# Kernel tuning notes

Hardware: AMD Instinct MI355X
Metric: run time of the kernel (lower is better)

The kernel has to match this reference:

```python
import jax, jax.numpy as jnp
import numpy as np

EPS = 1e-6
NUM_HEADS = 16


def _layernorm(x, g, b):
    m = jnp.mean(x, axis=-1, keepdims=True)
    v = jnp.mean(jnp.square(x - m), axis=-1, keepdims=True)
    return (x - m) * jax.lax.rsqrt(v + EPS) * g + b


def setup_inputs() -> dict:
    key = jax.random.key(0)
    ks = jax.random.split(key, 16)
    B, Lq, Lkv, D = 2, 2048, 4096, 2048
    Hd = D // NUM_HEADS
    s = 0.02
    return {
        "hidden_states": jax.random.normal(ks[0], (B, Lq, D), jnp.float32),
        "cross_attention_states": jax.random.normal(ks[1], (B, Lkv, D), jnp.float32),
        "q_w": jax.random.normal(ks[2], (D, D), jnp.float32) * s,
        "q_b": jnp.zeros((D,), jnp.float32),
        "k_w": jax.random.normal(ks[3], (D, D), jnp.float32) * s,
        "k_b": jnp.zeros((D,), jnp.float32),
        "v_w": jax.random.normal(ks[4], (D, D), jnp.float32) * s,
        "v_b": jnp.zeros((D,), jnp.float32),
        "o_w": jax.random.normal(ks[5], (D, D), jnp.float32) * s,
        "o_b": jnp.zeros((D,), jnp.float32),
        "qn_g": jnp.ones((Hd,), jnp.float32),
        "qn_b": jnp.zeros((Hd,), jnp.float32),
        "kn_g": jnp.ones((Hd,), jnp.float32),
        "kn_b": jnp.zeros((Hd,), jnp.float32),
    }


def reference(hidden_states, cross_attention_states,
              q_w, q_b, k_w, k_b, v_w, v_b, o_w, o_b,
              qn_g, qn_b, kn_g, kn_b):
    B, Lq, D = hidden_states.shape
    H = NUM_HEADS
    Hd = D // H
    scale = Hd ** -0.5

    # torch Linear: y = x @ W^T + b
    q = hidden_states @ q_w.T + q_b                        # [B,Lq,D]
    k = cross_attention_states @ k_w.T + k_b               # [B,Lkv,D]
    v = cross_attention_states @ v_w.T + v_b               # [B,Lkv,D]

    q = q.reshape(B, Lq, H, Hd).transpose(0, 2, 1, 3)      # [B,H,Lq,Hd]
    k = k.reshape(B, -1, H, Hd).transpose(0, 2, 1, 3)      # [B,H,Lkv,Hd]
    v = v.reshape(B, -1, H, Hd).transpose(0, 2, 1, 3)      # [B,H,Lkv,Hd]

    # per-head QK LayerNorm before scores
    q = _layernorm(q, qn_g, qn_b)
    k = _layernorm(k, kn_g, kn_b)

    attn_weights = jnp.einsum('bhqd,bhkd->bhqk', q, k) * scale
    attn_weights = jax.nn.softmax(attn_weights.astype(jnp.float32), axis=-1).astype(q.dtype)
    # dropout p=0.0 (inference) -> identity

    attn_output = jnp.einsum('bhqk,bhkd->bhqd', attn_weights, v)
    attn_output = attn_output.transpose(0, 2, 1, 3).reshape(B, Lq, D)
    attn_output = attn_output @ o_w.T + o_b
    return attn_output, attn_weights
```

## Files before the change

### kernel.cpp

```cpp
#include <hip/hip_runtime.h>
#include <cstdint>
#include <cstddef>

using u16 = unsigned short;
using f32x4 = __attribute__((ext_vector_type(4))) float;
using bf8   = __attribute__((ext_vector_type(8))) short;
using u32x4 = __attribute__((ext_vector_type(4))) unsigned;

#define DEVFN __device__ __forceinline__

constexpr int BB  = 2;
constexpr int LQ  = 2048;
constexpr int LKV = 4096;
constexpr int DD  = 2048;
constexpr int NH  = 16;
constexpr int HDm = 128;
constexpr float ATTN_SCALE = 0.08838834764831845f;
constexpr float LN_EPS = 1e-6f;
constexpr float LOG2E  = 1.4426950408889634f;
constexpr float SHIFT2 = 17.312340490667562f;

DEVFN u16 f2bf(float f) {
  unsigned u = __builtin_bit_cast(unsigned, f);
  u += 0x7fffu + ((u >> 16) & 1u);
  return (u16)(u >> 16);
}
DEVFN float bf2f(u16 h) { return __builtin_bit_cast(float, (unsigned)h << 16); }
DEVFN f32x4 mfma16(bf8 a, bf8 b, f32x4 c) {
  return __builtin_amdgcn_mfma_f32_16x16x32_bf16(a, b, c, 0, 0, 0);
}
DEVFN void gl16(const void* g, void* l) {
  __builtin_amdgcn_global_load_lds(
      (const __attribute__((address_space(1))) void*)g,
      (__attribute__((address_space(3))) void*)l, 16, 0, 0);
}
DEVFN void barrier_hard() {
  __builtin_amdgcn_s_barrier();
  __builtin_amdgcn_sched_barrier(0);
}

struct C6 {
  const float4* s[6];
  ushort4* d[6];
  unsigned off[7];
};
__global__ __launch_bounds__(256) void k_cvt6(C6 a) {
  unsigned gi = blockIdx.x * 256 + threadIdx.x;
  if (gi >= a.off[6]) return;
  int seg = 0;
#pragma unroll
  for (int i = 1; i < 6; ++i) seg += (gi >= a.off[i]);
  unsigned j = gi - a.off[seg];
  float4 v = a.s[seg][j];
  ushort4 o;
  o.x = f2bf(v.x); o.y = f2bf(v.y); o.z = f2bf(v.z); o.w = f2bf(v.w);
  a.d[seg][j] = o;
}

template <int MODE>
DEVFN void gemm_body(const u16* __restrict__ X, const u16* __restrict__ Wt,
                     const float* __restrict__ bias,
                     const float* __restrict__ lng, const float* __restrict__ lnb,
                     void* __restrict__ Y, int M, int N, int K,
                     int m0, int n0, u16* Sh, float (*Sm)[128], float (*Sq)[128]) {
  u16* As = Sh;
  u16* Bs = Sh + 128 * 64;
  const int tid = threadIdx.x;
  const int w = tid >> 6, l = tid & 63;
  const int wr = w >> 1, wc = w & 1;
  const int lr = l & 15, lk = (l >> 4) * 8;
  const int rsw = (l & 7) << 3;
  const int srow = l >> 3;
  const int scb = (l & 7) * 16;
  f32x4 acc[4][4] = {};

  for (int k0 = 0; k0 < K; k0 += 64) {
#pragma unroll
    for (int i = 0; i < 4; ++i) {
      int rbase = w * 32 + i * 8;
      int row = rbase + srow;
      int cb = scb ^ ((row & 7) << 4);
      gl16((const char*)&X[(size_t)(m0 + row) * K + k0] + cb, &As[rbase * 64]);
      gl16((const char*)&Wt[(size_t)(n0 + row) * K + k0] + cb, &Bs[rbase * 64]);
    }
    __syncthreads();
    bf8 af[4][2], bfr[4][2];
#pragma unroll
    for (int mi = 0; mi < 4; ++mi)
#pragma unroll
      for (int kk = 0; kk < 2; ++kk)
        af[mi][kk] = *(const bf8*)&As[(wr * 64 + mi * 16 + lr) * 64 + ((kk * 32 + lk) ^ rsw)];
#pragma unroll
    for (int ni = 0; ni < 4; ++ni)
#pragma unroll
      for (int kk = 0; kk < 2; ++kk)
        bfr[ni][kk] = *(const bf8*)&Bs[(wc * 64 + ni * 16 + lr) * 64 + ((kk * 32 + lk) ^ rsw)];
#pragma unroll
    for (int kk = 0; kk < 2; ++kk)
#pragma unroll
      for (int mi = 0; mi < 4; ++mi)
#pragma unroll
        for (int ni = 0; ni < 4; ++ni)
          acc[mi][ni] = mfma16(af[mi][kk], bfr[ni][kk], acc[mi][ni]);
    __syncthreads();
  }
  const int lrg = (l >> 4) * 4;

  float bv[4];
#pragma unroll
  for (int ni = 0; ni < 4; ++ni) bv[ni] = bias[n0 + wc * 64 + ni * 16 + lr];
#pragma unroll
  for (int mi = 0; mi < 4; ++mi)
#pragma unroll
    for (int ni = 0; ni < 4; ++ni)
#pragma unroll
      for (int r = 0; r < 4; ++r) acc[mi][ni][r] += bv[ni];

  if constexpr (MODE == 2 || MODE == 3) {
#pragma unroll
    for (int mi = 0; mi < 4; ++mi) {
#pragma unroll
      for (int r = 0; r < 4; ++r) {
        float ps = 0.f, pq = 0.f;
#pragma unroll
        for (int ni = 0; ni < 4; ++ni) {
          float v = acc[mi][ni][r];
          ps += v; pq += v * v;
        }
#pragma unroll
        for (int m = 1; m < 16; m <<= 1) {
          ps += __shfl_xor(ps, m);
          pq += __shfl_xor(pq, m);
        }
        if (lr == 0) {
          int rl = wr * 64 + mi * 16 + lrg + r;
          Sm[wc][rl] = ps; Sq[wc][rl] = pq;
        }
      }
    }
    __syncthreads();
    float gv[4], bbv[4];
#pragma unroll
    for (int ni = 0; ni < 4; ++ni) {
      int c = wc * 64 + ni * 16 + lr;
      gv[ni] = lng[c]; bbv[ni] = lnb[c];
    }
#pragma unroll
    for (int mi = 0; mi < 4; ++mi)
#pragma unroll
      for (int r = 0; r < 4; ++r) {
        int rl = wr * 64 + mi * 16 + lrg + r;
        float mean = (Sm[0][rl] + Sm[1][rl]) * (1.f / 128.f);
        float var  = (Sq[0][rl] + Sq[1][rl]) * (1.f / 128.f) - mean * mean;
        float rs = rsqrtf(var + LN_EPS);
#pragma unroll
        for (int ni = 0; ni < 4; ++ni) {
          float o = (acc[mi][ni][r] - mean) * rs * gv[ni] + bbv[ni];
          if (MODE == 3) o *= ATTN_SCALE;
          acc[mi][ni][r] = o;
        }
      }
  }

  if constexpr (MODE == 4) {
    u16* T = Sh;
#pragma unroll
    for (int mi = 0; mi < 4; ++mi)
#pragma unroll
      for (int ni = 0; ni < 4; ++ni)
#pragma unroll
        for (int r = 0; r < 4; ++r) {
          int mrow = wr * 64 + mi * 16 + lrg + r;
          int ncol = wc * 64 + ni * 16 + lr;
          T[mrow * 128 + (ncol ^ ((mrow & 7) << 3))] = f2bf(acc[mi][ni][r]);
        }
    __syncthreads();
    int hd = tid >> 1, half = tid & 1;
    int bq = m0 >> 12;
    int kvb = (m0 & (LKV - 1)) + half * 64;
    int hh = n0 >> 7;
    u16* vout = (u16*)Y + ((size_t)(bq * NH + hh) * HDm + hd) * LKV + kvb;
#pragma unroll
    for (int j8 = 0; j8 < 8; ++j8) {
      u16 tmp[8] __attribute__((aligned(16)));
#pragma unroll
      for (int j = 0; j < 8; ++j) {
        int kv = half * 64 + j8 * 8 + j;
        tmp[j] = T[kv * 128 + (hd ^ ((kv & 7) << 3))];
      }
      *(int4*)&vout[j8 * 8] = *(const int4*)tmp;
    }
    return;
  }

#pragma unroll
  for (int ni = 0; ni < 4; ++ni) {
    int n = n0 + wc * 64 + ni * 16 + lr;
#pragma unroll
    for (int mi = 0; mi < 4; ++mi) {
      int mb = m0 + wr * 64 + mi * 16 + lrg;
#pragma unroll
      for (int r = 0; r < 4; ++r) {
        float v = acc[mi][ni][r];
        if constexpr (MODE == 1)
          __builtin_nontemporal_store(v, &((float*)Y)[(size_t)(mb + r) * N + n]);
        else
          ((u16*)Y)[(size_t)(mb + r) * N + n] = f2bf(v);
      }
    }
  }
}

__global__ __launch_bounds__(256) void k_qkv(const u16* __restrict__ hsb,
                                             const u16* __restrict__ casb,
                                             const u16* __restrict__ qwb,
                                             const u16* __restrict__ kwb,
                                             const u16* __restrict__ vwb,
                                             const float* __restrict__ q_b,
                                             const float* __restrict__ k_b,
                                             const float* __restrict__ v_b,
                                             const float* __restrict__ qn_g,
                                             const float* __restrict__ qn_b,
                                             const float* __restrict__ kn_g,
                                             const float* __restrict__ kn_b,
                                             u16* __restrict__ Qp,
                                             u16* __restrict__ Kp,
                                             u16* __restrict__ Vtp) {
  __shared__ __align__(16) u16 Sh[2 * 128 * 64];
  __shared__ float Sm[2][128], Sq[2][128];
  const int bx = blockIdx.x;
  if (bx < 512) {
    int m0 = (bx & 31) << 7, n0 = (bx >> 5) << 7;
    gemm_body<3>(hsb, qwb, q_b, qn_g, qn_b, Qp, BB * LQ, DD, DD, m0, n0, Sh, Sm, Sq);
  } else if (bx < 1536) {
    int i = bx - 512;
    int m0 = (i & 63) << 7, n0 = (i >> 6) << 7;
    gemm_body<2>(casb, kwb, k_b, kn_g, kn_b, Kp, BB * LKV, DD, DD, m0, n0, Sh, Sm, Sq);
  } else {
    int i = bx - 1536;
    int m0 = (i & 63) << 7, n0 = (i >> 6) << 7;
    gemm_body<4>(casb, vwb, v_b, nullptr, nullptr, Vtp, BB * LKV, DD, DD, m0, n0, Sh, Sm, Sq);
  }
}

template <int MODE>
__global__ __launch_bounds__(256) void k_gemm_nt(const u16* __restrict__ X,
                                                 const u16* __restrict__ Wt,
                                                 const float* __restrict__ bias,
                                                 const float* __restrict__ lng,
                                                 const float* __restrict__ lnb,
                                                 void* __restrict__ Y,
                                                 int M, int N, int K) {
  __shared__ __align__(16) u16 Sh[2 * 128 * 64];
  __shared__ float Sm[2][128], Sq[2][128];
  gemm_body<MODE>(X, Wt, bias, lng, lnb, Y, M, N, K,
                  blockIdx.x * 128, blockIdx.y * 128, Sh, Sm, Sq);
}

__global__ __launch_bounds__(512, 4) void k_attn(const u16* __restrict__ Qp,
                                                 const u16* __restrict__ Kp,
                                                 const u16* __restrict__ Vt,
                                                 float* __restrict__ Wout,
                                                 u16* __restrict__ AO) {
  const int g = blockIdx.x;
  const int work = (g & 7) * 64 + (g >> 3);
  const int bh = work >> 4;
  const int b = bh >> 4, h = bh & 15;
  const int q0 = (work & 15) * 128;
  const int tid = threadIdx.x, w = tid >> 6, l = tid & 63;
  const int lr = l & 15, lk = (l >> 4) * 8;
  const int gq = l >> 4;
  const int rsw = (l & 7) << 3;
  __shared__ __align__(16) u16 Ks[2][64 * 128];
  __shared__ __align__(16) u16 Vs[2][128 * 64];

  bf8 qf[4];
  {
    const u16* qb = &Qp[((size_t)b * LQ + q0 + w * 16 + lr) * DD + h * HDm];
#pragma unroll
    for (int kc = 0; kc < 4; ++kc) qf[kc] = *(const bf8*)(qb + kc * 32 + lk);
  }
  const u16* Kb = Kp + (size_t)b * LKV * DD + h * HDm;
  const u16* Vb = Vt + (size_t)bh * HDm * LKV;

  auto stageK128 = [&](u16* buf, int kv0) {
#pragma unroll
    for (int i = 0; i < 4; ++i) {
      int rbase = i * 32 + w * 4;
      int row = rbase + (l >> 4);
      int cb = ((l & 15) * 16) ^ ((row & 7) << 4);
      gl16((const char*)(Kb + (size_t)(kv0 + row) * DD) + cb, &buf[rbase * 128]);
    }
  };
  auto stageK = [&](int buf, int kv0) {
#pragma unroll
    for (int i = 0; i < 2; ++i) {
      int rbase = i * 32 + w * 4;
      int row = rbase + (l >> 4);
      int cb = ((l & 15) * 16) ^ ((row & 7) << 4);
      gl16((const char*)(Kb + (size_t)(kv0 + row) * DD) + cb, &Ks[buf][rbase * 128]);
    }
  };
  auto stageV = [&](int buf, int kv0) {
#pragma unroll
    for (int i = 0; i < 2; ++i) {
      int rbase = i * 64 + w * 8;
      int row = rbase + (l >> 3);
      int cb = ((l & 7) * 16) ^ ((row & 7) << 4);
      gl16((const char*)(Vb + (size_t)row * LKV + kv0) + cb, &Vs[buf][rbase * 64]);
    }
  };

  u16* bufA0 = &Ks[0][0];
  u16* bufA1 = &Vs[0][0];
  float lsum = 0.f;
  stageK128(bufA0, 0);
  asm volatile("s_waitcnt vmcnt(0)" ::: "memory");
  barrier_hard();
  for (int t = 0; t < 32; ++t) {
    const u16* kb = (t & 1) ? bufA1 : bufA0;
    if (t < 31) stageK128((t & 1) ? bufA0 : bufA1, (t + 1) * 128);
    f32x4 s8[8];
    __builtin_amdgcn_s_setprio(1);
#pragma unroll
    for (int ni = 0; ni < 8; ++ni) {
      s8[ni] = f32x4{0.f, 0.f, 0.f, 0.f};
#pragma unroll
      for (int kc = 0; kc < 4; ++kc) {
        bf8 kf = *(const bf8*)&kb[(ni * 16 + lr) * 128 + ((kc * 32 + lk) ^ rsw)];
        s8[ni] = mfma16(kf, qf[kc], s8[ni]);
      }
    }
    __builtin_amdgcn_s_setprio(0);
#pragma unroll
    for (int ni = 0; ni < 8; ++ni)
#pragma unroll
      for (int r = 0; r < 4; ++r)
        lsum += exp2f(fmaf(s8[ni][r], LOG2E, -SHIFT2));
    asm volatile("s_waitcnt vmcnt(0)" ::: "memory");
    barrier_hard();
  }
  lsum += __shfl_xor(lsum, 16);
  lsum += __shfl_xor(lsum, 32);
  const float cr = -(SHIFT2 + __log2f(lsum));

  f32x4 oacc[8] = {};
  float* wq = Wout + ((size_t)bh * LQ + q0 + w * 16 + lr) * LKV;
  const int srcA = lr + ((gq & 1) << 5);
  const int srcB = srcA + 16;
  const bool hi = (gq >> 1) != 0;

  stageK(0, 0); stageV(0, 0);
  asm volatile("s_waitcnt vmcnt(0)" ::: "memory");
  barrier_hard();
  for (int t = 0; t < 64; ++t) {
    const int cur = t & 1;
    const int kv0 = t * 64;
    if (t < 63) { stageK(cur ^ 1, kv0 + 64); stageV(cur ^ 1, kv0 + 64); }
    f32x4 s[4];
    __builtin_amdgcn_s_setprio(1);
#pragma unroll
    for (int ni = 0; ni < 4; ++ni) {
      s[ni] = f32x4{0.f, 0.f, 0.f, 0.f};
#pragma unroll
      for (int kc = 0; kc < 4; ++kc) {
        bf8 kf = *(const bf8*)&Ks[cur][(ni * 16 + lr) * 128 + ((kc * 32 + lk) ^ rsw)];
        s[ni] = mfma16(kf, qf[kc], s[ni]);
      }
    }
    __builtin_amdgcn_s_setprio(0);
    unsigned pk2[4][2];
#pragma unroll
    for (int ni = 0; ni < 4; ++ni) {
      float p0 = exp2f(fmaf(s[ni][0], LOG2E, cr));
      float p1 = exp2f(fmaf(s[ni][1], LOG2E, cr));
      float p2 = exp2f(fmaf(s[ni][2], LOG2E, cr));
      float p3 = exp2f(fmaf(s[ni][3], LOG2E, cr));
      f32x4 pv4 = {p0, p1, p2, p3};
      __builtin_nontemporal_store(pv4, (f32x4*)(wq + kv0 + ni * 16 + 4 * gq));
      pk2[ni][0] = (unsigned)f2bf(p0) | ((unsigned)f2bf(p1) << 16);
      pk2[ni][1] = (unsigned)f2bf(p2) | ((unsigned)f2bf(p3) << 16);
    }
#pragma unroll
    for (int kk = 0; kk < 2; ++kk) {
      unsigned xa0 = __shfl(pk2[2 * kk][0], srcA), xa1 = __shfl(pk2[2 * kk][1], srcA);
      unsigned ya0 = __shfl(pk2[2 * kk + 1][0], srcA), ya1 = __shfl(pk2[2 * kk + 1][1], srcA);
      unsigned xb0 = __shfl(pk2[2 * kk][0], srcB), xb1 = __shfl(pk2[2 * kk][1], srcB);
      unsigned yb0 = __shfl(pk2[2 * kk + 1][0], srcB), yb1 = __shfl(pk2[2 * kk + 1][1], srcB);
      u32x4 pf32 = { hi ? ya0 : xa0, hi ? ya1 : xa1, hi ? yb0 : xb0, hi ? yb1 : xb1 };
      bf8 pf = __builtin_bit_cast(bf8, pf32);
      __builtin_amdgcn_s_setprio(1);
#pragma unroll
      for (int c = 0; c < 8; ++c) {
        bf8 vf = *(const bf8*)&Vs[cur][(c * 16 + lr) * 64 + ((kk * 32 + lk) ^ rsw)];
        oacc[c] = mfma16(pf, vf, oacc[c]);
      }
      __builtin_amdgcn_s_setprio(0);
    }
    asm volatile("s_waitcnt vmcnt(4)" ::: "memory");
    barrier_hard();
  }

#pragma unroll
  for (int c = 0; c < 8; ++c)
#pragma unroll
    for (int r = 0; r < 4; ++r)
      AO[((size_t)b * LQ + q0 + w * 16 + 4 * gq + r) * DD + h * HDm + c * 16 + lr] =
          f2bf(oacc[c][r]);
}

extern "C" void kernel_launch(void* const* d_in, const int* in_sizes, int n_in,
                              void* d_out, int out_size, void* d_ws, size_t ws_size,
                              hipStream_t stream) {
  const float* hs   = (const float*)d_in[0];
  const float* cas  = (const float*)d_in[1];
  const float* q_w  = (const float*)d_in[2];
  const float* q_b  = (const float*)d_in[3];
  const float* k_w  = (const float*)d_in[4];
  const float* k_b  = (const float*)d_in[5];
  const float* v_w  = (const float*)d_in[6];
  const float* v_b  = (const float*)d_in[7];
  const float* o_w  = (const float*)d_in[8];
  const float* o_b  = (const float*)d_in[9];
  const float* qn_g = (const float*)d_in[10];
  const float* qn_b = (const float*)d_in[11];
  const float* kn_g = (const float*)d_in[12];
  const float* kn_b = (const float*)d_in[13];

  float* out_attn = (float*)d_out;
  float* out_w    = out_attn + (size_t)BB * LQ * DD;

  constexpr size_t SZ_Q  = (size_t)BB * LQ * DD * 2;
  constexpr size_t SZ_KV = (size_t)BB * LKV * DD * 2;
  constexpr size_t SZ_W  = (size_t)DD * DD * 2;
  char* p = (char*)d_ws;
  u16* hsb  = (u16*)p;              p += SZ_Q;
  u16* casb = (u16*)p;              p += SZ_KV;
  u16* qwb  = (u16*)p;              p += SZ_W;
  u16* kwb  = (u16*)p;              p += SZ_W;
  u16* vwb  = (u16*)p;              p += SZ_W;
  u16* owb  = (u16*)p;              p += SZ_W;
  u16* Qp   = (u16*)p;              p += SZ_Q;
  u16* Kp   = (u16*)p;              p += SZ_KV;
  u16* Vtp  = (u16*)p;              p += SZ_KV;
  u16* AO   = (u16*)p;              p += SZ_Q;

  constexpr unsigned HS4 = BB * LQ * DD / 4;
  constexpr unsigned CAS4 = BB * LKV * DD / 4;
  constexpr unsigned W4 = DD * DD / 4;
  C6 a;
  a.s[0] = (const float4*)hs;  a.d[0] = (ushort4*)hsb;
  a.s[1] = (const float4*)cas; a.d[1] = (ushort4*)casb;
  a.s[2] = (const float4*)q_w; a.d[2] = (ushort4*)qwb;
  a.s[3] = (const float4*)k_w; a.d[3] = (ushort4*)kwb;
  a.s[4] = (const float4*)v_w; a.d[4] = (ushort4*)vwb;
  a.s[5] = (const float4*)o_w; a.d[5] = (ushort4*)owb;
  a.off[0] = 0;
  a.off[1] = HS4;
  a.off[2] = HS4 + CAS4;
  a.off[3] = HS4 + CAS4 + W4;
  a.off[4] = HS4 + CAS4 + 2 * W4;
  a.off[5] = HS4 + CAS4 + 3 * W4;
  a.off[6] = HS4 + CAS4 + 4 * W4;
  k_cvt6<<<dim3((a.off[6] + 255) / 256), dim3(256), 0, stream>>>(a);

  k_qkv<<<dim3(2560), dim3(256), 0, stream>>>(
      hsb, casb, qwb, kwb, vwb, q_b, k_b, v_b,
      qn_g, qn_b, kn_g, kn_b, Qp, Kp, Vtp);

  k_attn<<<dim3(LQ / 128 * BB * NH), dim3(512), 0, stream>>>(Qp, Kp, Vtp, out_w, AO);

  k_gemm_nt<1><<<dim3(BB * LQ / 128, DD / 128), dim3(256), 0, stream>>>(
      AO, owb, o_b, nullptr, nullptr, out_attn, BB * LQ, DD, DD);
}
```

Baseline: 743.0 us.

## Split sum-of-exp pass across wave pairs sharing K fragments over two query tiles

In the first (row-sum) pass, each wave now computes scores for two 16-row query tiles against half of each 128-key chunk, so every K fragment loaded from LDS feeds two MFMAs instead of one. This halves LDS reads of K per MFMA in the softmax-normaliser pass. Partial sums are combined across wave pairs through a small shared buffer and an extra block barrier. It costs more registers for the second Q fragment set, which may pressure occupancy under the 512x4 launch bounds.

Result: no change. 740.5 us (median of 2 runs) (-0.3%).

```diff
diff --git a/kernel.cpp b/kernel.cpp
--- a/kernel.cpp
+++ b/kernel.cpp
@@ -273,12 +273,17 @@
   const int rsw = (l & 7) << 3;
   __shared__ __align__(16) u16 Ks[2][64 * 128];
   __shared__ __align__(16) u16 Vs[2][128 * 64];
-
-  bf8 qf[4];
+  __shared__ float AsumS[8][2][16];
+
+  bf8 qfA[2][4];
   {
-    const u16* qb = &Qp[((size_t)b * LQ + q0 + w * 16 + lr) * DD + h * HDm];
-#pragma unroll
-    for (int kc = 0; kc < 4; ++kc) qf[kc] = *(const bf8*)(qb + kc * 32 + lk);
+    const int prow = (w >> 1) * 32;
+#pragma unroll
+    for (int qc = 0; qc < 2; ++qc) {
+      const u16* qb = &Qp[((size_t)b * LQ + q0 + prow + qc * 16 + lr) * DD + h * HDm];
+#pragma unroll
+      for (int kc = 0; kc < 4; ++kc) qfA[qc][kc] = *(const bf8*)(qb + kc * 32 + lk);
+    }
   }
   const u16* Kb = Kp + (size_t)b * LKV * DD + h * HDm;
   const u16* Vb = Vt + (size_t)bh * HDm * LKV;
@@ -313,36 +318,44 @@
 
   u16* bufA0 = &Ks[0][0];
   u16* bufA1 = &Vs[0][0];
-  float lsum = 0.f;
+  const int kvo = (w & 1) * 64;
+  float lsum0 = 0.f, lsum1 = 0.f;
   stageK128(bufA0, 0);
   asm volatile("s_waitcnt vmcnt(0)" ::: "memory");
   barrier_hard();
   for (int t = 0; t < 32; ++t) {
     const u16* kb = (t & 1) ? bufA1 : bufA0;
     if (t < 31) stageK128((t & 1) ? bufA0 : bufA1, (t + 1) * 128);
-    f32x4 s8[8];
-    __builtin_amdgcn_s_setprio(1);
-#pragma unroll
-    for (int ni = 0; ni < 8; ++ni) {
-      s8[ni] = f32x4{0.f, 0.f, 0.f, 0.f};
+#pragma unroll
+    for (int ni = 0; ni < 4; ++ni) {
+      f32x4 s0 = {0.f, 0.f, 0.f, 0.f}, s1 = {0.f, 0.f, 0.f, 0.f};
+      __builtin_amdgcn_s_setprio(1);
 #pragma unroll
       for (int kc = 0; kc < 4; ++kc) {
-        bf8 kf = *(const bf8*)&kb[(ni * 16 + lr) * 128 + ((kc * 32 + lk) ^ rsw)];
-        s8[ni] = mfma16(kf, qf[kc], s8[ni]);
-      }
-    }
-    __builtin_amdgcn_s_setprio(0);
-#pragma unroll
-    for (int ni = 0; ni < 8; ++ni)
-#pragma unroll
-      for (int r = 0; r < 4; ++r)
-        lsum += exp2f(fmaf(s8[ni][r], LOG2E, -SHIFT2));
+        bf8 kf = *(const bf8*)&kb[(kvo + ni * 16 + lr) * 128 + ((kc * 32 + lk) ^ rsw)];
+        s0 = mfma16(kf, qfA[0][kc], s0);
+        s1 = mfma16(kf, qfA[1][kc], s1);
+      }
+      __builtin_amdgcn_s_setprio(0);
+#pragma unroll
+      for (int r = 0; r < 4; ++r) {
+        lsum0 += exp2f(fmaf(s0[r], LOG2E, -SHIFT2));
+        lsum1 += exp2f(fmaf(s1[r], LOG2E, -SHIFT2));
+      }
+    }
     asm volatile("s_waitcnt vmcnt(0)" ::: "memory");
     barrier_hard();
   }
-  lsum += __shfl_xor(lsum, 16);
-  lsum += __shfl_xor(lsum, 32);
-  const float cr = -(SHIFT2 + __log2f(lsum));
+  lsum0 += __shfl_xor(lsum0, 16); lsum0 += __shfl_xor(lsum0, 32);
+  lsum1 += __shfl_xor(lsum1, 16); lsum1 += __shfl_xor(lsum1, 32);
+  if (l < 16) { AsumS[w][0][l] = lsum0; AsumS[w][1][l] = lsum1; }
+  __syncthreads();
+  float mine = (w & 1) ? lsum1 : lsum0;
+  float tot = mine + AsumS[w ^ 1][w & 1][lr];
+  const float cr = -(SHIFT2 + __log2f(tot));
+  bf8 qf[4];
+#pragma unroll
+  for (int kc = 0; kc < 4; ++kc) qf[kc] = (w & 1) ? qfA[1][kc] : qfA[0][kc];
 
   f32x4 oacc[8] = {};
   float* wq = Wout + ((size_t)bh * LQ + q0 + w * 16 + lr) * LKV;
```
